# Performance work log

Measured on AMD Instinct MI355X. Metric: run time of the kernel, lower is better.

Reference implementation:

```python
import jax, jax.numpy as jnp
import numpy as np

B, CIN, H, W = 16, 256, 48, 48
K, CD, MULTI = 64, 64, 1
GAMMA = (1.0 - 1e-10) ** (1.0 ** 0.6)  # iter = 1


def _ln(v, s, b, eps=1e-5):
    m = v.mean(-1, keepdims=True)
    var = ((v - m) ** 2).mean(-1, keepdims=True)
    return (v - m) / jnp.sqrt(var + eps) * s + b


def _spatial_masks():
    # pairwise squared distance between (i,j) grid coords, N = H*W
    ii, jj = jnp.meshgrid(jnp.arange(H, dtype=jnp.float32), jnp.arange(W, dtype=jnp.float32), indexing='ij')
    coord = jnp.stack([ii.ravel(), jj.ravel()], axis=1)  # [N,2]
    sq = (coord ** 2).sum(-1, keepdims=True)             # [N,1]
    d2 = sq - 2.0 * (coord @ coord.T) + sq.T             # [N,N]
    m = jnp.exp(-jnp.sqrt(jnp.abs(d2)))
    A = m / m.sum(0, keepdims=True)  # column-normalized (torch sums dim=1 of [B,N,N])
    cur, out = A, []
    for _ in range(MULTI):
        cur = cur @ A  # A^(num+2)
        out.append(cur)
    return out


def setup_inputs() -> dict:
    key = jax.random.key(0)
    ks = jax.random.split(key, 3)
    x = jax.random.normal(ks[0], (B, CIN, H, W), jnp.float32)
    clusters = jax.random.normal(ks[1], (1, K, CD), jnp.float32) * 0.1
    pi = jnp.ones((1, K), jnp.float32) / K
    cov = jnp.ones((1, K), jnp.float32)
    w_proj = jax.random.normal(ks[2], (CD, CIN), jnp.float32) / np.sqrt(CIN)
    nt_scale = jnp.ones((CD,), jnp.float32)
    nt_bias = jnp.zeros((CD,), jnp.float32)
    pn_scale = jnp.ones((K * MULTI,), jnp.float32)
    pn_bias = jnp.zeros((K * MULTI,), jnp.float32)
    return dict(x=x, clusters=clusters, pi=pi, cov=cov, w_proj=w_proj,
                nt_scale=nt_scale, nt_bias=nt_bias, pn_scale=pn_scale, pn_bias=pn_bias)


def reference(x, clusters, pi, cov, w_proj, nt_scale, nt_bias, pn_scale, pn_bias):
    N = H * W
    # 1x1 conv projection -> tokens [B,N,CD]
    xf = jnp.einsum('bihw,ci->bhwc', x, w_proj).reshape(B, N, CD)
    # normalized templates (batch-invariant)
    t = _ln(clusters[0], nt_scale, nt_bias)  # [K,CD]
    # squared euclidean distance via expansion (avoids [B,CD,N,K] intermediate)
    x2 = (xf ** 2).sum(-1)  # [B,N]
    t2 = (t ** 2).sum(-1)   # [K]
    d = x2[:, :, None] + t2[None, None, :] - 2.0 * jnp.einsum('bnc,kc->bnk', xf, t)
    logits = jnp.log(pi[0] / jnp.sqrt(cov[0])) - d / cov[0] / 2.0
    attn = jax.nn.softmax(logits, axis=-1)  # [B,N,K]
    # EM-style updates
    pi_new = pi + GAMMA * (attn.sum(1) / N - pi)                     # [B,K]
    attn_n = attn + 1e-8
    attn_n = attn_n / attn_n.sum(-2, keepdims=True)                  # normalize over N
    t_new = clusters + GAMMA * (jnp.einsum('bnc,bnk->bkc', xf, attn_n) - clusters)  # [B,K,CD]
    tn2 = (t_new ** 2).sum(-1)  # [B,K]
    d2 = x2[:, :, None] + tn2[:, None, :] - 2.0 * jnp.einsum('bnc,bkc->bnk', xf, t_new)
    cov_new = cov + GAMMA * ((d2 * attn_n).sum(1) - cov)             # [B,K]
    # spatial distance-encoding masks (stop-gradient / constant w.r.t. params)
    masks = _spatial_masks()
    outp = jnp.concatenate([jnp.einsum('bnk,nm->bkm', attn_n, M) for M in masks], axis=1)  # [B,K*MULTI,N]
    outp = _ln(outp.transpose(0, 2, 1), pn_scale, pn_bias).transpose(0, 2, 1)
    outp = outp.reshape(B, K * MULTI, H, W)
    attn_out = attn.transpose(0, 2, 1).reshape(B, K, H, W)
    return outp, attn_out, t_new, pi_new, cov_new
```

## Files before the change

kernel.cpp:

```cpp
#include <hip/hip_runtime.h>
#include <hip/hip_bf16.h>
#include <math.h>

#define B_   16
#define CIN_ 256
#define H_   48
#define W_   48
#define N_   2304
#define K_   64
#define CD_  64

#define GAMMA_F 0.9999999999f

using f32x4  = __attribute__((ext_vector_type(4))) float;
using bf16x8 = __attribute__((ext_vector_type(8))) short;
using s16x4  = __attribute__((ext_vector_type(4))) short;

__device__ __forceinline__ void split_bf(float x, short& hi, short& lo) {
  unsigned u = __builtin_bit_cast(unsigned, x);
  unsigned r = (u + 0x7FFFu + ((u >> 16) & 1u)) & 0xFFFF0000u;
  hi = (short)(r >> 16);
  float res = x - __builtin_bit_cast(float, r);
  unsigned u2 = __builtin_bit_cast(unsigned, res);
  unsigned r2 = u2 + 0x7FFFu + ((u2 >> 16) & 1u);
  lo = (short)(r2 >> 16);
}

constexpr size_t OFF_XF    = 0;
constexpr size_t OFF_ANT   = OFF_XF    + (size_t)B_*N_*CD_;
constexpr size_t OFF_T     = OFF_ANT   + (size_t)B_*K_*N_;
constexpr size_t OFF_T2    = OFF_T     + (size_t)K_*CD_;
constexpr size_t OFF_LOGPI = OFF_T2    + K_;
constexpr size_t OFF_I2C   = OFF_LOGPI + K_;
constexpr size_t OFF_X2    = OFF_I2C   + K_;
constexpr size_t OFF_CS    = OFF_X2    + (size_t)B_*N_;
constexpr size_t OFF_ICN   = OFF_CS    + (size_t)B_*K_;
constexpr size_t OFF_MASKH = OFF_ICN   + (size_t)B_*K_;
constexpr size_t OFF_MASKL = OFF_MASKH + (size_t)N_*N_/2;

constexpr size_t OUT_OUTP = 0;
constexpr size_t OUT_ATTN = (size_t)B_*K_*N_;
constexpr size_t OUT_TNEW = OUT_ATTN + (size_t)B_*K_*N_;
constexpr size_t OUT_PI   = OUT_TNEW + (size_t)B_*K_*CD_;
constexpr size_t OUT_COV  = OUT_PI   + (size_t)B_*K_;

__global__ __launch_bounds__(256) void k_proj(const float* __restrict__ x, const float* __restrict__ wp,
                                              float* __restrict__ xf) {
  __shared__ float xs[32][64];
  __shared__ float ws_[32][65];
  int b = blockIdx.y, n0 = blockIdx.x * 64;
  int tid = threadIdx.x;
  int nn = tid & 63, cg = tid >> 6;
  float acc[16];
#pragma unroll
  for (int j = 0; j < 16; j++) acc[j] = 0.f;
  for (int i0 = 0; i0 < CIN_; i0 += 32) {
#pragma unroll
    for (int j = 0; j < 8; j++) {
      int ii = cg * 8 + j;
      xs[ii][nn] = x[((size_t)b * CIN_ + i0 + ii) * N_ + n0 + nn];
    }
    {
      int c = tid >> 2, iq = (tid & 3) * 8;
#pragma unroll
      for (int j = 0; j < 8; j++)
        ws_[iq + j][c] = wp[(size_t)c * CIN_ + i0 + iq + j];
    }
    __syncthreads();
#pragma unroll
    for (int ii = 0; ii < 32; ++ii) {
      float xv = xs[ii][nn];
#pragma unroll
      for (int j = 0; j < 16; j++) acc[j] += xv * ws_[ii][cg * 16 + j];
    }
    __syncthreads();
  }
  float* dst = xf + ((size_t)b * N_ + n0 + nn) * CD_ + cg * 16;
#pragma unroll
  for (int j4 = 0; j4 < 4; j4++)
    *(float4*)(dst + j4 * 4) = make_float4(acc[j4*4], acc[j4*4+1], acc[j4*4+2], acc[j4*4+3]);
}

__global__ void k_templ(const float* __restrict__ clusters, const float* __restrict__ pi,
                        const float* __restrict__ cov, const float* __restrict__ nsc,
                        const float* __restrict__ nbi, float* __restrict__ t, float* __restrict__ t2,
                        float* __restrict__ logpi, float* __restrict__ i2c) {
  int k = threadIdx.x;
  float v[CD_];
  float m = 0;
#pragma unroll
  for (int c = 0; c < CD_; c++) { v[c] = clusters[k * CD_ + c]; m += v[c]; }
  m /= CD_;
  float var = 0;
#pragma unroll
  for (int c = 0; c < CD_; c++) { float d = v[c] - m; var += d * d; }
  var /= CD_;
  float inv = 1.f / sqrtf(var + 1e-5f);
  float s2 = 0;
#pragma unroll
  for (int c = 0; c < CD_; c++) {
    float tv = (v[c] - m) * inv * nsc[c] + nbi[c];
    t[k * CD_ + c] = tv;
    s2 += tv * tv;
  }
  t2[k] = s2;
  float p = pi[k], cv = cov[k];
  logpi[k] = logf(p) - 0.5f * logf(cv);
  i2c[k] = 0.5f / cv;
}

__global__ __launch_bounds__(256) void k_attn(const float* __restrict__ xf, const float* __restrict__ t,
                                              const float* __restrict__ t2, const float* __restrict__ logpi,
                                              const float* __restrict__ i2c,
                                              float* __restrict__ aout, float* __restrict__ x2o) {
  __shared__ __align__(16) float ts[K_][72];
  __shared__ float t2s[K_], lps[K_], ics[K_];
  int tid = threadIdx.x;
  for (int i = tid; i < K_ * CD_; i += 256) ts[i >> 6][i & 63] = t[i];
  if (tid < K_) { t2s[tid] = t2[tid]; lps[tid] = logpi[tid]; ics[tid] = i2c[tid]; }
  __syncthreads();
  int b = blockIdx.y;
  int tok = tid >> 2, kg = tid & 3;
  int n = blockIdx.x * 64 + tok;
  const float4* xr = (const float4*)(xf + ((size_t)b * N_ + n) * CD_);
  float4 xv[16];
#pragma unroll
  for (int i = 0; i < 16; i++) xv[i] = xr[i];
  float x2 = 0;
#pragma unroll
  for (int i = 0; i < 16; i++) x2 += xv[i].x * xv[i].x + xv[i].y * xv[i].y + xv[i].z * xv[i].z + xv[i].w * xv[i].w;
  if (kg == 0) x2o[(size_t)b * N_ + n] = x2;
  float lg[16];
#pragma unroll
  for (int kk = 0; kk < 16; kk++) {
    int k = kk * 4 + kg;
    const float4* tk = (const float4*)&ts[k][0];
    float d0 = 0, d1 = 0, d2 = 0, d3 = 0;
#pragma unroll
    for (int i = 0; i < 16; i += 4) {
      float4 t0 = tk[i], t1 = tk[i + 1], t2v = tk[i + 2], t3 = tk[i + 3];
      d0 += xv[i].x * t0.x + xv[i].y * t0.y + xv[i].z * t0.z + xv[i].w * t0.w;
      d1 += xv[i+1].x * t1.x + xv[i+1].y * t1.y + xv[i+1].z * t1.z + xv[i+1].w * t1.w;
      d2 += xv[i+2].x * t2v.x + xv[i+2].y * t2v.y + xv[i+2].z * t2v.z + xv[i+2].w * t2v.w;
      d3 += xv[i+3].x * t3.x + xv[i+3].y * t3.y + xv[i+3].z * t3.z + xv[i+3].w * t3.w;
    }
    float dot = (d0 + d1) + (d2 + d3);
    lg[kk] = lps[k] - (x2 + t2s[k] - 2.f * dot) * ics[k];
  }
  float mx = lg[0];
#pragma unroll
  for (int kk = 1; kk < 16; kk++) mx = fmaxf(mx, lg[kk]);
  mx = fmaxf(mx, __shfl_xor(mx, 1));
  mx = fmaxf(mx, __shfl_xor(mx, 2));
  float sum = 0;
#pragma unroll
  for (int kk = 0; kk < 16; kk++) { lg[kk] = __expf(lg[kk] - mx); sum += lg[kk]; }
  sum += __shfl_xor(sum, 1);
  sum += __shfl_xor(sum, 2);
  float inv = 1.f / sum;
  size_t base = (size_t)b * K_ * N_ + n;
#pragma unroll
  for (int kk = 0; kk < 16; kk++)
    aout[base + (size_t)(kk * 4 + kg) * N_] = lg[kk] * inv;
}

__global__ __launch_bounds__(256) void k_colsum2(const float* __restrict__ ant, float* __restrict__ colsum) {
  int r = blockIdx.x, tid = threadIdx.x;
  const float* row = ant + (size_t)r * N_;
  float s = 0;
  for (int n = tid; n < N_; n += 256) s += row[n];
#pragma unroll
  for (int off = 32; off; off >>= 1) s += __shfl_down(s, off);
  __shared__ float red[4];
  if ((tid & 63) == 0) red[tid >> 6] = s;
  __syncthreads();
  if (tid == 0) colsum[r] = red[0] + red[1] + red[2] + red[3];
}

__global__ void k_pinew(const float* __restrict__ colsum, const float* __restrict__ pi,
                        float* __restrict__ pi_out, float* __restrict__ icn) {
  int b = blockIdx.x, k = threadIdx.x;
  float cs = colsum[b * K_ + k];
  float p = pi[k];
  pi_out[b * K_ + k] = p + GAMMA_F * (cs / (float)N_ - p);
  icn[b * K_ + k] = 1.f / (cs + (float)N_ * 1e-8f);
}

__global__ __launch_bounds__(256) void k_tnew_cov(const float* __restrict__ ant, const float* __restrict__ icn,
                                                  const float* __restrict__ xf, const float* __restrict__ x2,
                                                  const float* __restrict__ clusters, const float* __restrict__ cov,
                                                  float* __restrict__ tnew_out, float* __restrict__ cov_out) {
  int k = blockIdx.x, b = blockIdx.y;
  int tid = threadIdx.x;
  int c = tid & 63, g = tid >> 6;
  const float* arow = ant + ((size_t)b * K_ + k) * N_;
  const float* x2r = x2 + (size_t)b * N_;
  float acc = 0, ax2 = 0;
#pragma unroll 4
  for (int n = g; n < N_; n += 4) {
    float a = arow[n] + 1e-8f;
    acc += a * xf[((size_t)b * N_ + n) * CD_ + c];
    ax2 += a * x2r[n];
  }
  __shared__ float red[4][64];
  __shared__ float red2[4];
  red[g][c] = acc;
  if (c == 0) red2[g] = ax2;
  __syncthreads();
  if (tid < 64) {
    float icnv = icn[b * K_ + k];
    float s = (red[0][c] + red[1][c] + red[2][c] + red[3][c]) * icnv;
    float cl = clusters[k * CD_ + c];
    float tv = cl + GAMMA_F * (s - cl);
    tnew_out[((size_t)b * K_ + k) * CD_ + c] = tv;
    float sq = tv * tv;
    float st = s * tv;
#pragma unroll
    for (int off = 32; off; off >>= 1) { sq += __shfl_down(sq, off); st += __shfl_down(st, off); }
    if (c == 0) {
      float ax2t = (red2[0] + red2[1] + red2[2] + red2[3]) * icnv;
      float cv = cov[k];
      float csum = ax2t + sq - 2.f * st;
      cov_out[b * K_ + k] = cv + GAMMA_F * (csum - cv);
    }
  }
}

__global__ __launch_bounds__(256) void k_acenter(const float* __restrict__ attn, const float* __restrict__ icn,
                                                 short* __restrict__ AcH, short* __restrict__ AcL) {
  int b = blockIdx.y;
  int n = blockIdx.x * 256 + threadIdx.x;
  const float* base = attn + (size_t)b * K_ * N_ + n;
  const float* ic = icn + b * K_;
  float a[K_];
  float s = 0;
#pragma unroll 8
  for (int k = 0; k < K_; k++) {
    a[k] = base[(size_t)k * N_];
    s += (a[k] + 1e-8f) * ic[k];
  }
  float amean = s * (1.f / (float)K_);
#pragma unroll 8
  for (int k = 0; k < K_; k++) {
    float icv = ic[k];
    float va = fmaf(a[k], icv, 1e-8f * icv) - amean;
    short h, l;
    split_bf(va, h, l);
    AcH[(size_t)(b * K_ + k) * N_ + n] = h;
    AcL[(size_t)(b * K_ + k) * N_ + n] = l;
  }
}

__global__ __launch_bounds__(256) void k_mask(short* __restrict__ MH, short* __restrict__ ML) {
  __shared__ float red[4];
  const int m = blockIdx.x;
  const int mi = m / W_, mj = m % W_;
  const int tid = threadIdx.x;
  float e[N_ / 256];
  float s = 0;
#pragma unroll
  for (int it = 0; it < N_ / 256; it++) {
    int n = it * 256 + tid;
    int ni = n / W_, nj = n - (n / W_) * W_;
    int dx = ni - mi, dy = nj - mj;
    e[it] = __expf(-sqrtf((float)(dx * dx + dy * dy)));
    s += e[it];
  }
#pragma unroll
  for (int off = 32; off; off >>= 1) s += __shfl_down(s, off);
  if ((tid & 63) == 0) red[tid >> 6] = s;
  __syncthreads();
  const float imc = 1.f / (red[0] + red[1] + red[2] + red[3]);
#pragma unroll
  for (int it = 0; it < N_ / 256; it++) {
    int n = it * 256 + tid;
    short h, l;
    split_bf(e[it] * imc, h, l);
    MH[(size_t)m * N_ + n] = h;
    ML[(size_t)m * N_ + n] = l;
  }
}


__global__ __launch_bounds__(256) void gemm1_mfma(const short* __restrict__ AcH, const short* __restrict__ AcL,
                                                  const short* __restrict__ MaskH, const short* __restrict__ MaskL,
                                                  short* __restrict__ YdH, short* __restrict__ YdL) {
  __shared__ __align__(16) short Ah[2][64][40];
  __shared__ __align__(16) short Al[2][64][40];
  __shared__ __align__(16) short Bh[2][64][40];
  __shared__ __align__(16) short Bl[2][64][40];
  const int tid = threadIdx.x;
  const int b = blockIdx.y;
  const int m0 = b * 64, n0 = blockIdx.x * 64;
  const int lane = tid & 63, w = tid >> 6;
  const int fr = lane & 15, quad = lane >> 4;
  const int srow = tid >> 2;
  const int skq  = (tid & 3) * 8;
  const size_t mrow = (size_t)(n0 + srow) * N_;
  const size_t abase = (size_t)(m0 + srow) * N_ + skq;
  f32x4 acc[4] = {};
  bf16x8 ah = *(const bf16x8*)&AcH[abase];
  bf16x8 al = *(const bf16x8*)&AcL[abase];
  bf16x8 mh = *(const bf16x8*)&MaskH[mrow + skq];
  bf16x8 ml = *(const bf16x8*)&MaskL[mrow + skq];
  for (int k0 = 0; k0 < N_; k0 += 32) {
    const int c = (k0 >> 5) & 1;
    *(bf16x8*)&Ah[c][srow][skq] = ah;
    *(bf16x8*)&Al[c][srow][skq] = al;
    *(bf16x8*)&Bh[c][srow][skq] = mh;
    *(bf16x8*)&Bl[c][srow][skq] = ml;
    if (k0 + 32 < N_) {
      ah = *(const bf16x8*)&AcH[abase + k0 + 32];
      al = *(const bf16x8*)&AcL[abase + k0 + 32];
      mh = *(const bf16x8*)&MaskH[mrow + k0 + 32 + skq];
      ml = *(const bf16x8*)&MaskL[mrow + k0 + 32 + skq];
    }
    __syncthreads();
    bf16x8 afh = *(const bf16x8*)&Ah[c][w * 16 + fr][quad * 8];
    bf16x8 afl = *(const bf16x8*)&Al[c][w * 16 + fr][quad * 8];
#pragma unroll
    for (int ns = 0; ns < 4; ns++) {
      bf16x8 bfh = *(const bf16x8*)&Bh[c][ns * 16 + fr][quad * 8];
      bf16x8 bfl = *(const bf16x8*)&Bl[c][ns * 16 + fr][quad * 8];
      acc[ns] = __builtin_amdgcn_mfma_f32_16x16x32_bf16(afh, bfh, acc[ns], 0, 0, 0);
      acc[ns] = __builtin_amdgcn_mfma_f32_16x16x32_bf16(afh, bfl, acc[ns], 0, 0, 0);
      acc[ns] = __builtin_amdgcn_mfma_f32_16x16x32_bf16(afl, bfh, acc[ns], 0, 0, 0);
    }
  }
  const size_t rbase = (size_t)(m0 + w * 16 + fr) * N_ + n0;
#pragma unroll
  for (int ns = 0; ns < 4; ns++) {
    s16x4 h4, l4;
#pragma unroll
    for (int reg = 0; reg < 4; reg++) { short h, l; split_bf(acc[ns][reg], h, l); h4[reg] = h; l4[reg] = l; }
    *(s16x4*)&YdH[rbase + ns * 16 + quad * 4] = h4;
    *(s16x4*)&YdL[rbase + ns * 16 + quad * 4] = l4;
  }
}

__global__ __launch_bounds__(256) void gemm2_ln_mfma(const short* __restrict__ YdH, const short* __restrict__ YdL,
                                                     const short* __restrict__ MaskH, const short* __restrict__ MaskL,
                                                     const float* __restrict__ pns, const float* __restrict__ pnb,
                                                     float* __restrict__ outp) {
  __shared__ __align__(16) short Ah[2][64][40];
  __shared__ __align__(16) short Al[2][64][40];
  __shared__ __align__(16) short Bh[2][64][40];
  __shared__ __align__(16) short Bl[2][64][40];
  __shared__ __align__(16) float S[64][68];
  __shared__ float rstd[64], sc[64], bi[64];
  const int tid = threadIdx.x;
  const int b = blockIdx.y;
  const int m0 = b * 64, n0 = blockIdx.x * 64;
  const int lane = tid & 63, w = tid >> 6;
  const int fr = lane & 15, quad = lane >> 4;
  const int srow = tid >> 2;
  const int skq  = (tid & 3) * 8;
  const size_t mrow = (size_t)(n0 + srow) * N_;
  if (tid < 64) { sc[tid] = pns[tid]; bi[tid] = pnb[tid]; }
  const size_t abase = (size_t)(m0 + srow) * N_ + skq;
  f32x4 acc[4] = {};
  bf16x8 yh = *(const bf16x8*)&YdH[abase];
  bf16x8 yl = *(const bf16x8*)&YdL[abase];
  bf16x8 mh = *(const bf16x8*)&MaskH[mrow + skq];
  bf16x8 ml = *(const bf16x8*)&MaskL[mrow + skq];
  for (int k0 = 0; k0 < N_; k0 += 32) {
    const int c = (k0 >> 5) & 1;
    *(bf16x8*)&Ah[c][srow][skq] = yh;
    *(bf16x8*)&Al[c][srow][skq] = yl;
    *(bf16x8*)&Bh[c][srow][skq] = mh;
    *(bf16x8*)&Bl[c][srow][skq] = ml;
    if (k0 + 32 < N_) {
      yh = *(const bf16x8*)&YdH[abase + k0 + 32];
      yl = *(const bf16x8*)&YdL[abase + k0 + 32];
      mh = *(const bf16x8*)&MaskH[mrow + k0 + 32 + skq];
      ml = *(const bf16x8*)&MaskL[mrow + k0 + 32 + skq];
    }
    __syncthreads();
    bf16x8 afh = *(const bf16x8*)&Ah[c][w * 16 + fr][quad * 8];
    bf16x8 afl = *(const bf16x8*)&Al[c][w * 16 + fr][quad * 8];
#pragma unroll
    for (int ns = 0; ns < 4; ns++) {
      bf16x8 bfh = *(const bf16x8*)&Bh[c][ns * 16 + fr][quad * 8];
      bf16x8 bfl = *(const bf16x8*)&Bl[c][ns * 16 + fr][quad * 8];
      acc[ns] = __builtin_amdgcn_mfma_f32_16x16x32_bf16(afh, bfh, acc[ns], 0, 0, 0);
      acc[ns] = __builtin_amdgcn_mfma_f32_16x16x32_bf16(afh, bfl, acc[ns], 0, 0, 0);
      acc[ns] = __builtin_amdgcn_mfma_f32_16x16x32_bf16(afl, bfh, acc[ns], 0, 0, 0);
    }
  }
  __syncthreads();
#pragma unroll
  for (int ns = 0; ns < 4; ns++)
    *(f32x4*)&S[w * 16 + fr][ns * 16 + quad * 4] = acc[ns];
  __syncthreads();
  if (tid < 64) {
    float ss = 0;
#pragma unroll
    for (int k = 0; k < K_; k++) { float d = S[k][tid]; ss += d * d; }
    rstd[tid] = 1.f / sqrtf(ss / (float)K_ + 1e-5f);
  }
  __syncthreads();
  {
    int c = tid & 63, g = tid >> 6;
#pragma unroll
    for (int i = 0; i < 16; i++) {
      int r = g * 16 + i;
      outp[(size_t)(m0 + r) * N_ + n0 + c] = S[r][c] * rstd[c] * sc[r] + bi[r];
    }
  }
}

extern "C" void kernel_launch(void* const* d_in, const int* in_sizes, int n_in,
                              void* d_out, int out_size, void* d_ws, size_t ws_size,
                              hipStream_t stream) {
  const float* x        = (const float*)d_in[0];
  const float* clusters = (const float*)d_in[1];
  const float* pi       = (const float*)d_in[2];
  const float* cov      = (const float*)d_in[3];
  const float* w_proj   = (const float*)d_in[4];
  const float* nt_scale = (const float*)d_in[5];
  const float* nt_bias  = (const float*)d_in[6];
  const float* pn_scale = (const float*)d_in[7];
  const float* pn_bias  = (const float*)d_in[8];
  float* out = (float*)d_out;
  float* w = (float*)d_ws;
  short* YdH = (short*)(w + OFF_XF);
  short* YdL = YdH + (size_t)B_ * K_ * N_;
  short* AcH = (short*)(w + OFF_ANT);
  short* AcL = AcH + (size_t)B_ * K_ * N_;
  short* MaskH = (short*)(w + OFF_MASKH);
  short* MaskL = (short*)(w + OFF_MASKL);
  float* attn = out + OUT_ATTN;

  k_mask<<<N_, 256, 0, stream>>>(MaskH, MaskL);
  k_proj<<<dim3(N_ / 64, B_), 256, 0, stream>>>(x, w_proj, w + OFF_XF);
  k_templ<<<1, K_, 0, stream>>>(clusters, pi, cov, nt_scale, nt_bias,
                                w + OFF_T, w + OFF_T2, w + OFF_LOGPI, w + OFF_I2C);
  k_attn<<<dim3(N_ / 64, B_), 256, 0, stream>>>(w + OFF_XF, w + OFF_T, w + OFF_T2,
                                                w + OFF_LOGPI, w + OFF_I2C,
                                                attn, w + OFF_X2);
  k_colsum2<<<B_ * K_, 256, 0, stream>>>(attn, w + OFF_CS);
  k_pinew<<<B_, K_, 0, stream>>>(w + OFF_CS, pi, out + OUT_PI, w + OFF_ICN);
  k_acenter<<<dim3(N_ / 256, B_), 256, 0, stream>>>(attn, w + OFF_ICN, AcH, AcL);
  k_tnew_cov<<<dim3(K_, B_), 256, 0, stream>>>(attn, w + OFF_ICN, w + OFF_XF, w + OFF_X2,
                                               clusters, cov, out + OUT_TNEW, out + OUT_COV);
  gemm1_mfma<<<dim3(N_ / 64, B_), 256, 0, stream>>>(AcH, AcL, MaskH, MaskL, YdH, YdL);
  gemm2_ln_mfma<<<dim3(N_ / 64, B_), 256, 0, stream>>>(YdH, YdL, MaskH, MaskL,
                                                       pn_scale, pn_bias, out + OUT_OUTP);
}
```

Baseline: 378.6 us.

## Load MFMA fragments directly from global memory, bypassing LDS staging

Both split-bf16 GEMM kernels stop staging the A and B tiles through double-buffered shared memory. Each lane now loads its MFMA fragments straight from global memory into registers and prefetches the next k-slice in registers. This removes the LDS writes and reads and the per-iteration __syncthreads. In exchange, the four waves each fetch the same mask (B) rows, which raises L1/L2 traffic and register pressure.

```diff
diff --git a/kernel.cpp b/kernel.cpp
--- a/kernel.cpp
+++ b/kernel.cpp
@@ -285,47 +285,43 @@
 __global__ __launch_bounds__(256) void gemm1_mfma(const short* __restrict__ AcH, const short* __restrict__ AcL,
                                                   const short* __restrict__ MaskH, const short* __restrict__ MaskL,
                                                   short* __restrict__ YdH, short* __restrict__ YdL) {
-  __shared__ __align__(16) short Ah[2][64][40];
-  __shared__ __align__(16) short Al[2][64][40];
-  __shared__ __align__(16) short Bh[2][64][40];
-  __shared__ __align__(16) short Bl[2][64][40];
   const int tid = threadIdx.x;
   const int b = blockIdx.y;
   const int m0 = b * 64, n0 = blockIdx.x * 64;
   const int lane = tid & 63, w = tid >> 6;
   const int fr = lane & 15, quad = lane >> 4;
-  const int srow = tid >> 2;
-  const int skq  = (tid & 3) * 8;
-  const size_t mrow = (size_t)(n0 + srow) * N_;
-  const size_t abase = (size_t)(m0 + srow) * N_ + skq;
+  const size_t arow = (size_t)(m0 + w * 16 + fr) * N_ + quad * 8;
+  size_t brow[4];
+#pragma unroll
+  for (int ns = 0; ns < 4; ns++) brow[ns] = (size_t)(n0 + ns * 16 + fr) * N_ + quad * 8;
   f32x4 acc[4] = {};
-  bf16x8 ah = *(const bf16x8*)&AcH[abase];
-  bf16x8 al = *(const bf16x8*)&AcL[abase];
-  bf16x8 mh = *(const bf16x8*)&MaskH[mrow + skq];
-  bf16x8 ml = *(const bf16x8*)&MaskL[mrow + skq];
+  bf16x8 ah = *(const bf16x8*)&AcH[arow];
+  bf16x8 al = *(const bf16x8*)&AcL[arow];
+  bf16x8 bh[4], bl[4];
+#pragma unroll
+  for (int ns = 0; ns < 4; ns++) {
+    bh[ns] = *(const bf16x8*)&MaskH[brow[ns]];
+    bl[ns] = *(const bf16x8*)&MaskL[brow[ns]];
+  }
   for (int k0 = 0; k0 < N_; k0 += 32) {
-    const int c = (k0 >> 5) & 1;
-    *(bf16x8*)&Ah[c][srow][skq] = ah;
-    *(bf16x8*)&Al[c][srow][skq] = al;
-    *(bf16x8*)&Bh[c][srow][skq] = mh;
-    *(bf16x8*)&Bl[c][srow][skq] = ml;
-    if (k0 + 32 < N_) {
-      ah = *(const bf16x8*)&AcH[abase + k0 + 32];
-      al = *(const bf16x8*)&AcL[abase + k0 + 32];
-      mh = *(const bf16x8*)&MaskH[mrow + k0 + 32 + skq];
-      ml = *(const bf16x8*)&MaskL[mrow + k0 + 32 + skq];
-    }
-    __syncthreads();
-    bf16x8 afh = *(const bf16x8*)&Ah[c][w * 16 + fr][quad * 8];
-    bf16x8 afl = *(const bf16x8*)&Al[c][w * 16 + fr][quad * 8];
+    const int kn = (k0 + 32 < N_) ? k0 + 32 : k0;
+    bf16x8 ah1 = *(const bf16x8*)&AcH[arow + kn];
+    bf16x8 al1 = *(const bf16x8*)&AcL[arow + kn];
+    bf16x8 bh1[4], bl1[4];
 #pragma unroll
     for (int ns = 0; ns < 4; ns++) {
-      bf16x8 bfh = *(const bf16x8*)&Bh[c][ns * 16 + fr][quad * 8];
-      bf16x8 bfl = *(const bf16x8*)&Bl[c][ns * 16 + fr][quad * 8];
-      acc[ns] = __builtin_amdgcn_mfma_f32_16x16x32_bf16(afh, bfh, acc[ns], 0, 0, 0);
-      acc[ns] = __builtin_amdgcn_mfma_f32_16x16x32_bf16(afh, bfl, acc[ns], 0, 0, 0);
-      acc[ns] = __builtin_amdgcn_mfma_f32_16x16x32_bf16(afl, bfh, acc[ns], 0, 0, 0);
-    }
+      bh1[ns] = *(const bf16x8*)&MaskH[brow[ns] + kn];
+      bl1[ns] = *(const bf16x8*)&MaskL[brow[ns] + kn];
+    }
+#pragma unroll
+    for (int ns = 0; ns < 4; ns++) {
+      acc[ns] = __builtin_amdgcn_mfma_f32_16x16x32_bf16(ah, bh[ns], acc[ns], 0, 0, 0);
+      acc[ns] = __builtin_amdgcn_mfma_f32_16x16x32_bf16(ah, bl[ns], acc[ns], 0, 0, 0);
+      acc[ns] = __builtin_amdgcn_mfma_f32_16x16x32_bf16(al, bh[ns], acc[ns], 0, 0, 0);
+    }
+    ah = ah1; al = al1;
+#pragma unroll
+    for (int ns = 0; ns < 4; ns++) { bh[ns] = bh1[ns]; bl[ns] = bl1[ns]; }
   }
   const size_t rbase = (size_t)(m0 + w * 16 + fr) * N_ + n0;
 #pragma unroll
@@ -342,10 +338,6 @@
                                                      const short* __restrict__ MaskH, const short* __restrict__ MaskL,
                                                      const float* __restrict__ pns, const float* __restrict__ pnb,
                                                      float* __restrict__ outp) {
-  __shared__ __align__(16) short Ah[2][64][40];
-  __shared__ __align__(16) short Al[2][64][40];
-  __shared__ __align__(16) short Bh[2][64][40];
-  __shared__ __align__(16) short Bl[2][64][40];
   __shared__ __align__(16) float S[64][68];
   __shared__ float rstd[64], sc[64], bi[64];
   const int tid = threadIdx.x;
@@ -353,41 +345,40 @@
   const int m0 = b * 64, n0 = blockIdx.x * 64;
   const int lane = tid & 63, w = tid >> 6;
   const int fr = lane & 15, quad = lane >> 4;
-  const int srow = tid >> 2;
-  const int skq  = (tid & 3) * 8;
-  const size_t mrow = (size_t)(n0 + srow) * N_;
   if (tid < 64) { sc[tid] = pns[tid]; bi[tid] = pnb[tid]; }
-  const size_t abase = (size_t)(m0 + srow) * N_ + skq;
+  const size_t arow = (size_t)(m0 + w * 16 + fr) * N_ + quad * 8;
+  size_t brow[4];
+#pragma unroll
+  for (int ns = 0; ns < 4; ns++) brow[ns] = (size_t)(n0 + ns * 16 + fr) * N_ + quad * 8;
   f32x4 acc[4] = {};
-  bf16x8 yh = *(const bf16x8*)&YdH[abase];
-  bf16x8 yl = *(const bf16x8*)&YdL[abase];
-  bf16x8 mh = *(const bf16x8*)&MaskH[mrow + skq];
-  bf16x8 ml = *(const bf16x8*)&MaskL[mrow + skq];
+  bf16x8 yh = *(const bf16x8*)&YdH[arow];
+  bf16x8 yl = *(const bf16x8*)&YdL[arow];
+  bf16x8 bh[4], bl[4];
+#pragma unroll
+  for (int ns = 0; ns < 4; ns++) {
+    bh[ns] = *(const bf16x8*)&MaskH[brow[ns]];
+    bl[ns] = *(const bf16x8*)&MaskL[brow[ns]];
+  }
   for (int k0 = 0; k0 < N_; k0 += 32) {
-    const int c = (k0 >> 5) & 1;
-    *(bf16x8*)&Ah[c][srow][skq] = yh;
-    *(bf16x8*)&Al[c][srow][skq] = yl;
-    *(bf16x8*)&Bh[c][srow][skq] = mh;
-    *(bf16x8*)&Bl[c][srow][skq] = ml;
-    if (k0 + 32 < N_) {
-      yh = *(const bf16x8*)&YdH[abase + k0 + 32];
-      yl = *(const bf16x8*)&YdL[abase + k0 + 32];
-      mh = *(const bf16x8*)&MaskH[mrow + k0 + 32 + skq];
-      ml = *(const bf16x8*)&MaskL[mrow + k0 + 32 + skq];
-    }
-    __syncthreads();
-    bf16x8 afh = *(const bf16x8*)&Ah[c][w * 16 + fr][quad * 8];
-    bf16x8 afl = *(const bf16x8*)&Al[c][w * 16 + fr][quad * 8];
+    const int kn = (k0 + 32 < N_) ? k0 + 32 : k0;
+    bf16x8 yh1 = *(const bf16x8*)&YdH[arow + kn];
+    bf16x8 yl1 = *(const bf16x8*)&YdL[arow + kn];
+    bf16x8 bh1[4], bl1[4];
 #pragma unroll
     for (int ns = 0; ns < 4; ns++) {
-      bf16x8 bfh = *(const bf16x8*)&Bh[c][ns * 16 + fr][quad * 8];
-      bf16x8 bfl = *(const bf16x8*)&Bl[c][ns * 16 + fr][quad * 8];
-      acc[ns] = __builtin_amdgcn_mfma_f32_16x16x32_bf16(afh, bfh, acc[ns], 0, 0, 0);
-      acc[ns] = __builtin_amdgcn_mfma_f32_16x16x32_bf16(afh, bfl, acc[ns], 0, 0, 0);
-      acc[ns] = __builtin_amdgcn_mfma_f32_16x16x32_bf16(afl, bfh, acc[ns], 0, 0, 0);
-    }
-  }
-  __syncthreads();
+      bh1[ns] = *(const bf16x8*)&MaskH[brow[ns] + kn];
+      bl1[ns] = *(const bf16x8*)&MaskL[brow[ns] + kn];
+    }
+#pragma unroll
+    for (int ns = 0; ns < 4; ns++) {
+      acc[ns] = __builtin_amdgcn_mfma_f32_16x16x32_bf16(yh, bh[ns], acc[ns], 0, 0, 0);
+      acc[ns] = __builtin_amdgcn_mfma_f32_16x16x32_bf16(yh, bl[ns], acc[ns], 0, 0, 0);
+      acc[ns] = __builtin_amdgcn_mfma_f32_16x16x32_bf16(yl, bh[ns], acc[ns], 0, 0, 0);
+    }
+    yh = yh1; yl = yl1;
+#pragma unroll
+    for (int ns = 0; ns < 4; ns++) { bh[ns] = bh1[ns]; bl[ns] = bl1[ns]; }
+  }
 #pragma unroll
   for (int ns = 0; ns < 4; ns++)
     *(f32x4*)&S[w * 16 + fr][ns * 16 + quad * 4] = acc[ns];
```

Result: slower. 717.3 us (+89.5%).

## Split-K the two mask GEMMs and combine partials in separate kernels

Applied to the files above, without the earlier changes.

Both large mask GEMMs now split the N-long reduction into two halves via a third grid dimension, which doubles the block count from 576 to 1152. Each block writes an fp32 partial, and separate combine kernels sum the halves: the first re-splits into bf16 hi/lo, the second applies the layer norm. Warps are also rearranged into a 2x2 layout of 32x32 sub-tiles for better fragment reuse. Buffers are reused: the xf workspace and the output region hold the partials, and Yd aliases the Ac buffers. The cost is extra fp32 partial traffic and two more launches.

```diff
diff --git a/kernel.cpp b/kernel.cpp
--- a/kernel.cpp
+++ b/kernel.cpp
@@ -11,6 +11,7 @@
 #define CD_  64
 
 #define GAMMA_F 0.9999999999f
+#define KSPLIT 1152
 
 using f32x4  = __attribute__((ext_vector_type(4))) float;
 using bf16x8 = __attribute__((ext_vector_type(8))) short;
@@ -282,115 +283,109 @@
 }
 
 
-__global__ __launch_bounds__(256) void gemm1_mfma(const short* __restrict__ AcH, const short* __restrict__ AcL,
-                                                  const short* __restrict__ MaskH, const short* __restrict__ MaskL,
-                                                  short* __restrict__ YdH, short* __restrict__ YdL) {
+template<int GEMM>
+__global__ __launch_bounds__(256) void gemm_splitk(const short* __restrict__ AH, const short* __restrict__ AL,
+                                                   const short* __restrict__ MaskH, const short* __restrict__ MaskL,
+                                                   float* __restrict__ P0, float* __restrict__ P1) {
   __shared__ __align__(16) short Ah[2][64][40];
   __shared__ __align__(16) short Al[2][64][40];
   __shared__ __align__(16) short Bh[2][64][40];
   __shared__ __align__(16) short Bl[2][64][40];
   const int tid = threadIdx.x;
   const int b = blockIdx.y;
+  const int z = blockIdx.z;
   const int m0 = b * 64, n0 = blockIdx.x * 64;
   const int lane = tid & 63, w = tid >> 6;
   const int fr = lane & 15, quad = lane >> 4;
+  const int wr = (w >> 1) * 32;
+  const int wc = (w & 1) * 32;
   const int srow = tid >> 2;
   const int skq  = (tid & 3) * 8;
+  const int zb = z * KSPLIT;
   const size_t mrow = (size_t)(n0 + srow) * N_;
   const size_t abase = (size_t)(m0 + srow) * N_ + skq;
-  f32x4 acc[4] = {};
-  bf16x8 ah = *(const bf16x8*)&AcH[abase];
-  bf16x8 al = *(const bf16x8*)&AcL[abase];
-  bf16x8 mh = *(const bf16x8*)&MaskH[mrow + skq];
-  bf16x8 ml = *(const bf16x8*)&MaskL[mrow + skq];
-  for (int k0 = 0; k0 < N_; k0 += 32) {
-    const int c = (k0 >> 5) & 1;
+  f32x4 acc[2][2] = {};
+  bf16x8 ah = *(const bf16x8*)&AH[abase + zb];
+  bf16x8 al = *(const bf16x8*)&AL[abase + zb];
+  bf16x8 mh = *(const bf16x8*)&MaskH[mrow + zb + skq];
+  bf16x8 ml = *(const bf16x8*)&MaskL[mrow + zb + skq];
+  for (int it = 0; it < KSPLIT / 32; ++it) {
+    const int c = it & 1;
     *(bf16x8*)&Ah[c][srow][skq] = ah;
     *(bf16x8*)&Al[c][srow][skq] = al;
     *(bf16x8*)&Bh[c][srow][skq] = mh;
     *(bf16x8*)&Bl[c][srow][skq] = ml;
-    if (k0 + 32 < N_) {
-      ah = *(const bf16x8*)&AcH[abase + k0 + 32];
-      al = *(const bf16x8*)&AcL[abase + k0 + 32];
-      mh = *(const bf16x8*)&MaskH[mrow + k0 + 32 + skq];
-      ml = *(const bf16x8*)&MaskL[mrow + k0 + 32 + skq];
+    if (it + 1 < KSPLIT / 32) {
+      const int kn = zb + (it + 1) * 32;
+      ah = *(const bf16x8*)&AH[abase + kn];
+      al = *(const bf16x8*)&AL[abase + kn];
+      mh = *(const bf16x8*)&MaskH[mrow + kn + skq];
+      ml = *(const bf16x8*)&MaskL[mrow + kn + skq];
     }
     __syncthreads();
-    bf16x8 afh = *(const bf16x8*)&Ah[c][w * 16 + fr][quad * 8];
-    bf16x8 afl = *(const bf16x8*)&Al[c][w * 16 + fr][quad * 8];
-#pragma unroll
-    for (int ns = 0; ns < 4; ns++) {
-      bf16x8 bfh = *(const bf16x8*)&Bh[c][ns * 16 + fr][quad * 8];
-      bf16x8 bfl = *(const bf16x8*)&Bl[c][ns * 16 + fr][quad * 8];
-      acc[ns] = __builtin_amdgcn_mfma_f32_16x16x32_bf16(afh, bfh, acc[ns], 0, 0, 0);
-      acc[ns] = __builtin_amdgcn_mfma_f32_16x16x32_bf16(afh, bfl, acc[ns], 0, 0, 0);
-      acc[ns] = __builtin_amdgcn_mfma_f32_16x16x32_bf16(afl, bfh, acc[ns], 0, 0, 0);
-    }
-  }
-  const size_t rbase = (size_t)(m0 + w * 16 + fr) * N_ + n0;
-#pragma unroll
-  for (int ns = 0; ns < 4; ns++) {
+    bf16x8 afh[2], afl[2], bfh[2], bfl[2];
+#pragma unroll
+    for (int i = 0; i < 2; i++) {
+      afh[i] = *(const bf16x8*)&Ah[c][wr + i * 16 + fr][quad * 8];
+      afl[i] = *(const bf16x8*)&Al[c][wr + i * 16 + fr][quad * 8];
+      bfh[i] = *(const bf16x8*)&Bh[c][wc + i * 16 + fr][quad * 8];
+      bfl[i] = *(const bf16x8*)&Bl[c][wc + i * 16 + fr][quad * 8];
+    }
+#pragma unroll
+    for (int i = 0; i < 2; i++)
+#pragma unroll
+      for (int j = 0; j < 2; j++) {
+        acc[i][j] = __builtin_amdgcn_mfma_f32_16x16x32_bf16(afh[i], bfh[j], acc[i][j], 0, 0, 0);
+        acc[i][j] = __builtin_amdgcn_mfma_f32_16x16x32_bf16(afh[i], bfl[j], acc[i][j], 0, 0, 0);
+        acc[i][j] = __builtin_amdgcn_mfma_f32_16x16x32_bf16(afl[i], bfh[j], acc[i][j], 0, 0, 0);
+      }
+  }
+  float* P = z ? P1 : P0;
+#pragma unroll
+  for (int i = 0; i < 2; i++)
+#pragma unroll
+    for (int j = 0; j < 2; j++)
+      *(f32x4*)&P[(size_t)(m0 + wr + i * 16 + fr) * N_ + n0 + wc + j * 16 + quad * 4] = acc[i][j];
+}
+
+__global__ __launch_bounds__(256) void k_combine1(const float* __restrict__ P0, const float* __restrict__ P1,
+                                                  short* __restrict__ YdH, short* __restrict__ YdL) {
+  const int b = blockIdx.y, n0 = blockIdx.x * 64;
+  const int tid = threadIdx.x;
+  const int row = tid >> 2, coff = (tid & 3) * 16;
+  const size_t base = (size_t)(b * 64 + row) * N_ + n0 + coff;
+#pragma unroll
+  for (int q = 0; q < 4; q++) {
+    float4 a = *(const float4*)&P0[base + q * 4];
+    float4 d = *(const float4*)&P1[base + q * 4];
     s16x4 h4, l4;
-#pragma unroll
-    for (int reg = 0; reg < 4; reg++) { short h, l; split_bf(acc[ns][reg], h, l); h4[reg] = h; l4[reg] = l; }
-    *(s16x4*)&YdH[rbase + ns * 16 + quad * 4] = h4;
-    *(s16x4*)&YdL[rbase + ns * 16 + quad * 4] = l4;
-  }
-}
-
-__global__ __launch_bounds__(256) void gemm2_ln_mfma(const short* __restrict__ YdH, const short* __restrict__ YdL,
-                                                     const short* __restrict__ MaskH, const short* __restrict__ MaskL,
+    short h, l;
+    split_bf(a.x + d.x, h, l); h4[0] = h; l4[0] = l;
+    split_bf(a.y + d.y, h, l); h4[1] = h; l4[1] = l;
+    split_bf(a.z + d.z, h, l); h4[2] = h; l4[2] = l;
+    split_bf(a.w + d.w, h, l); h4[3] = h; l4[3] = l;
+    *(s16x4*)&YdH[base + q * 4] = h4;
+    *(s16x4*)&YdL[base + q * 4] = l4;
+  }
+}
+
+__global__ __launch_bounds__(256) void k_combine2_ln(const float* __restrict__ Q0, const float* __restrict__ Q1,
                                                      const float* __restrict__ pns, const float* __restrict__ pnb,
                                                      float* __restrict__ outp) {
-  __shared__ __align__(16) short Ah[2][64][40];
-  __shared__ __align__(16) short Al[2][64][40];
-  __shared__ __align__(16) short Bh[2][64][40];
-  __shared__ __align__(16) short Bl[2][64][40];
   __shared__ __align__(16) float S[64][68];
   __shared__ float rstd[64], sc[64], bi[64];
+  const int b = blockIdx.y, n0 = blockIdx.x * 64;
   const int tid = threadIdx.x;
-  const int b = blockIdx.y;
-  const int m0 = b * 64, n0 = blockIdx.x * 64;
-  const int lane = tid & 63, w = tid >> 6;
-  const int fr = lane & 15, quad = lane >> 4;
-  const int srow = tid >> 2;
-  const int skq  = (tid & 3) * 8;
-  const size_t mrow = (size_t)(n0 + srow) * N_;
+  const int m0 = b * 64;
   if (tid < 64) { sc[tid] = pns[tid]; bi[tid] = pnb[tid]; }
-  const size_t abase = (size_t)(m0 + srow) * N_ + skq;
-  f32x4 acc[4] = {};
-  bf16x8 yh = *(const bf16x8*)&YdH[abase];
-  bf16x8 yl = *(const bf16x8*)&YdL[abase];
-  bf16x8 mh = *(const bf16x8*)&MaskH[mrow + skq];
-  bf16x8 ml = *(const bf16x8*)&MaskL[mrow + skq];
-  for (int k0 = 0; k0 < N_; k0 += 32) {
-    const int c = (k0 >> 5) & 1;
-    *(bf16x8*)&Ah[c][srow][skq] = yh;
-    *(bf16x8*)&Al[c][srow][skq] = yl;
-    *(bf16x8*)&Bh[c][srow][skq] = mh;
-    *(bf16x8*)&Bl[c][srow][skq] = ml;
-    if (k0 + 32 < N_) {
-      yh = *(const bf16x8*)&YdH[abase + k0 + 32];
-      yl = *(const bf16x8*)&YdL[abase + k0 + 32];
-      mh = *(const bf16x8*)&MaskH[mrow + k0 + 32 + skq];
-      ml = *(const bf16x8*)&MaskL[mrow + k0 + 32 + skq];
-    }
-    __syncthreads();
-    bf16x8 afh = *(const bf16x8*)&Ah[c][w * 16 + fr][quad * 8];
-    bf16x8 afl = *(const bf16x8*)&Al[c][w * 16 + fr][quad * 8];
-#pragma unroll
-    for (int ns = 0; ns < 4; ns++) {
-      bf16x8 bfh = *(const bf16x8*)&Bh[c][ns * 16 + fr][quad * 8];
-      bf16x8 bfl = *(const bf16x8*)&Bl[c][ns * 16 + fr][quad * 8];
-      acc[ns] = __builtin_amdgcn_mfma_f32_16x16x32_bf16(afh, bfh, acc[ns], 0, 0, 0);
-      acc[ns] = __builtin_amdgcn_mfma_f32_16x16x32_bf16(afh, bfl, acc[ns], 0, 0, 0);
-      acc[ns] = __builtin_amdgcn_mfma_f32_16x16x32_bf16(afl, bfh, acc[ns], 0, 0, 0);
-    }
-  }
-  __syncthreads();
-#pragma unroll
-  for (int ns = 0; ns < 4; ns++)
-    *(f32x4*)&S[w * 16 + fr][ns * 16 + quad * 4] = acc[ns];
+  const int row = tid >> 2, coff = (tid & 3) * 16;
+  const size_t base = (size_t)(m0 + row) * N_ + n0 + coff;
+#pragma unroll
+  for (int q = 0; q < 4; q++) {
+    float4 a = *(const float4*)&Q0[base + q * 4];
+    float4 d = *(const float4*)&Q1[base + q * 4];
+    *(f32x4*)&S[row][coff + q * 4] = f32x4{a.x + d.x, a.y + d.y, a.z + d.z, a.w + d.w};
+  }
   __syncthreads();
   if (tid < 64) {
     float ss = 0;
@@ -423,13 +418,15 @@
   const float* pn_bias  = (const float*)d_in[8];
   float* out = (float*)d_out;
   float* w = (float*)d_ws;
-  short* YdH = (short*)(w + OFF_XF);
-  short* YdL = YdH + (size_t)B_ * K_ * N_;
   short* AcH = (short*)(w + OFF_ANT);
   short* AcL = AcH + (size_t)B_ * K_ * N_;
+  short* YdH = AcH;
+  short* YdL = AcL;
   short* MaskH = (short*)(w + OFF_MASKH);
   short* MaskL = (short*)(w + OFF_MASKL);
   float* attn = out + OUT_ATTN;
+  float* Phalf0 = w + OFF_XF;
+  float* Phalf1 = out + OUT_OUTP;
 
   k_mask<<<N_, 256, 0, stream>>>(MaskH, MaskL);
   k_proj<<<dim3(N_ / 64, B_), 256, 0, stream>>>(x, w_proj, w + OFF_XF);
@@ -443,7 +440,8 @@
   k_acenter<<<dim3(N_ / 256, B_), 256, 0, stream>>>(attn, w + OFF_ICN, AcH, AcL);
   k_tnew_cov<<<dim3(K_, B_), 256, 0, stream>>>(attn, w + OFF_ICN, w + OFF_XF, w + OFF_X2,
                                                clusters, cov, out + OUT_TNEW, out + OUT_COV);
-  gemm1_mfma<<<dim3(N_ / 64, B_), 256, 0, stream>>>(AcH, AcL, MaskH, MaskL, YdH, YdL);
-  gemm2_ln_mfma<<<dim3(N_ / 64, B_), 256, 0, stream>>>(YdH, YdL, MaskH, MaskL,
-                                                       pn_scale, pn_bias, out + OUT_OUTP);
-}
+  gemm_splitk<1><<<dim3(N_ / 64, B_, 2), 256, 0, stream>>>(AcH, AcL, MaskH, MaskL, Phalf0, Phalf1);
+  k_combine1<<<dim3(N_ / 64, B_), 256, 0, stream>>>(Phalf0, Phalf1, YdH, YdL);
+  gemm_splitk<2><<<dim3(N_ / 64, B_, 2), 256, 0, stream>>>(YdH, YdL, MaskH, MaskL, Phalf0, Phalf1);
+  k_combine2_ln<<<dim3(N_ / 64, B_), 256, 0, stream>>>(Phalf0, Phalf1, pn_scale, pn_bias, out + OUT_OUTP);
+}
```

Result: faster. 361.9 us (-4.4%).
